# Kernel tuning notes

Measured on AMD Instinct MI355X. Metric: run time of the kernel, lower is better.

## Reference

```python
import jax, jax.numpy as jnp
import numpy as np

EPS = 1e-5

def layer_norm(x, g, b):
    m = x.mean(-1, keepdims=True)
    v = ((x - m) ** 2).mean(-1, keepdims=True)
    return (x - m) * jax.lax.rsqrt(v + EPS) * g + b

def setup_inputs() -> dict:
    key = jax.random.key(0)
    ks = jax.random.split(key, 8)
    H, T = 512, 256
    hidden_states = jax.random.normal(ks[0], (1, T, H), jnp.float32)
    U = jax.random.normal(ks[1], (H, H), jnp.float32) * 0.01
    W = jax.random.normal(ks[2], (H, H), jnp.float32) * 0.01
    a = jax.random.normal(ks[3], (H,), jnp.float32) * 0.01
    b = jax.random.normal(ks[4], (H,), jnp.float32) * 0.01
    gamma = jnp.ones((H,), jnp.float32)
    beta = jnp.zeros((H,), jnp.float32)
    targets = jax.random.randint(ks[5], (T,), 0, H)  # deterministic stand-in for torch.randint dummy targets
    return {"hidden_states": hidden_states, "U": U, "W": W, "a": a, "b": b,
            "gamma": gamma, "beta": beta, "targets": targets}

def reference(hidden_states, U, W, a, b, gamma, beta, targets):
    # batch must be 1 (torch.outer in the original requires 1-D vectors)
    h = hidden_states[0]                      # (T, H)
    z = jax.nn.relu(h @ U + a)                # (T, H) slow-path hidden

    # Per-timestep grads of CE(LayerNorm(z_t @ W + b), target_t) w.r.t. W, b
    def step_loss(z_t, tgt, W_, b_):
        y = layer_norm(z_t @ W_ + b_, gamma, beta)
        return -jax.nn.log_softmax(y)[tgt]
    grad_fn = jax.grad(step_loss, argnums=(2, 3))
    gradW, gradb = jax.vmap(grad_fn, in_axes=(0, 0, None, None))(z, targets, W, b)  # (T,H,H), (T,H)

    # W_update_t[p,q] = sum_{i<t} h_i[p] * h_t[q] * gradW_i[p,q]
    G = h[:, :, None] * gradW                 # (T, H, H)
    A = jnp.cumsum(G, axis=0) - G             # exclusive prefix sum over i
    W_upd = A * h[:, None, :]                 # (T, H, H)
    fastW = W - jnp.cumsum(W_upd, axis=0)     # cumulative fast weights per t

    # b_update_t[q] = h_t[q] * sum_{i<t} (sum_p h_i[p]) * gradb_i[q]
    c = h.sum(-1)                             # (T,)
    Bc = c[:, None] * gradb                   # (T, H)
    Bex = jnp.cumsum(Bc, axis=0) - Bc         # exclusive
    b_upd = h * Bex
    fastb = b - jnp.cumsum(b_upd, axis=0)     # (T, H)

    pre = jnp.einsum('th,thq->tq', z, fastW) + fastb
    out = layer_norm(pre, gamma, beta)        # (T, H)
    return out[None]                          # (1, T, H)
```

## Files before the change

kernel.cpp:

```cpp
#include <hip/hip_runtime.h>

#define T 256
#define H 512
#define EPSF 1e-5f

__device__ __forceinline__ float block_sum(float v, float* s4) {
    for (int o = 32; o; o >>= 1) v += __shfl_xor(v, o);
    int w = threadIdx.x >> 6;
    __syncthreads();
    if ((threadIdx.x & 63) == 0) s4[w] = v;
    __syncthreads();
    return s4[0] + s4[1] + s4[2] + s4[3];
}

__device__ __forceinline__ float block_max(float v, float* s4) {
    for (int o = 32; o; o >>= 1) v = fmaxf(v, __shfl_xor(v, o));
    int w = threadIdx.x >> 6;
    __syncthreads();
    if ((threadIdx.x & 63) == 0) s4[w] = v;
    __syncthreads();
    return fmaxf(fmaxf(s4[0], s4[1]), fmaxf(s4[2], s4[3]));
}

__device__ __forceinline__ float bsum16(float v, float* s16) {
    for (int o = 32; o; o >>= 1) v += __shfl_xor(v, o);
    int w = threadIdx.x >> 6;
    __syncthreads();
    if ((threadIdx.x & 63) == 0) s16[w] = v;
    __syncthreads();
    float r = 0.f;
    #pragma unroll
    for (int i = 0; i < 16; ++i) r += s16[i];
    return r;
}

__global__ __launch_bounds__(256) void k1(
        const float* __restrict__ h, const float* __restrict__ U,
        const float* __restrict__ a, float* __restrict__ Z,
        float* __restrict__ HZ, float* __restrict__ c) {
    int bid = blockIdx.x, tid = threadIdx.x;
    int lane = tid & 63, w = tid >> 6;
    int t0 = (bid >> 2) * 2, qt = bid & 3;
    __shared__ __align__(16) float sh[1024];
    __shared__ float2 part[3][2][64];
    ((float4*)sh)[tid] = ((const float4*)(h + t0 * H))[tid];
    __syncthreads();

    if (qt == 0 && w < 2) {
        float s = 0.f;
        #pragma unroll
        for (int j = 0; j < 8; ++j) s += sh[w * 512 + lane + j * 64];
        for (int o = 32; o; o >>= 1) s += __shfl_xor(s, o);
        if (lane == 0) c[t0 + w] = s;
    }

    int qc = qt * 64 + lane;
    const float2* U2 = (const float2*)U;
    float2 acc0 = {0.f, 0.f}, acc1 = {0.f, 0.f};
    int kbeg = w * 128;
    for (int k0 = kbeg; k0 < kbeg + 128; k0 += 8) {
        float2 bv[8];
        #pragma unroll
        for (int u = 0; u < 8; ++u) bv[u] = U2[(k0 + u) * 256 + qc];
        float a0[8], a1[8];
        #pragma unroll
        for (int u = 0; u < 8; ++u) { a0[u] = sh[k0 + u]; a1[u] = sh[512 + k0 + u]; }
        #pragma unroll
        for (int u = 0; u < 8; ++u) {
            acc0.x += a0[u] * bv[u].x; acc0.y += a0[u] * bv[u].y;
            acc1.x += a1[u] * bv[u].x; acc1.y += a1[u] * bv[u].y;
        }
    }
    if (w) { part[w - 1][0][lane] = acc0; part[w - 1][1][lane] = acc1; }
    __syncthreads();
    if (w == 0) {
        #pragma unroll
        for (int p = 0; p < 3; ++p) {
            acc0.x += part[p][0][lane].x; acc0.y += part[p][0][lane].y;
            acc1.x += part[p][1][lane].x; acc1.y += part[p][1][lane].y;
        }
        float2 av = ((const float2*)a)[qc];
        float z0x = fmaxf(acc0.x + av.x, 0.f), z0y = fmaxf(acc0.y + av.y, 0.f);
        float z1x = fmaxf(acc1.x + av.x, 0.f), z1y = fmaxf(acc1.y + av.y, 0.f);
        float2 h0 = ((float2*)sh)[qc], h1 = ((float2*)sh)[256 + qc];
        ((float2*)Z)[t0 * 256 + qc]        = make_float2(z0x, z0y);
        ((float2*)Z)[(t0 + 1) * 256 + qc]  = make_float2(z1x, z1y);
        ((float2*)HZ)[t0 * 256 + qc]       = make_float2(h0.x * z0x, h0.y * z0y);
        ((float2*)HZ)[(t0 + 1) * 256 + qc] = make_float2(h1.x * z1x, h1.y * z1y);
    }
}

__global__ __launch_bounds__(256) void k2(
        const float* __restrict__ h, const float* __restrict__ Z,
        const float* __restrict__ W, const float* __restrict__ bb,
        const float* __restrict__ HZ, const float* __restrict__ c,
        float* __restrict__ u0, float* __restrict__ Beta,
        float* __restrict__ S) {
    __shared__ __align__(16) float smem[2 * 8 * 516 + 256];
    int bid = blockIdx.x, tid = threadIdx.x;
    int lane = tid & 63, w = tid >> 6;
    if (bid < 512) {
        float* sh = smem;
        float2* part = (float2*)(smem + 1024);
        int t0 = (bid >> 2) * 2, qt = bid & 3;
        ((float4*)sh)[tid] = ((const float4*)(Z + t0 * H))[tid];
        __syncthreads();
        int qc = qt * 64 + lane;
        const float2* W2 = (const float2*)W;
        float2 acc0 = {0.f, 0.f}, acc1 = {0.f, 0.f};
        int kbeg = w * 128;
        for (int k0 = kbeg; k0 < kbeg + 128; k0 += 8) {
            float2 bv[8];
            #pragma unroll
            for (int u = 0; u < 8; ++u) bv[u] = W2[(k0 + u) * 256 + qc];
            float a0[8], a1[8];
            #pragma unroll
            for (int u = 0; u < 8; ++u) { a0[u] = sh[k0 + u]; a1[u] = sh[512 + k0 + u]; }
            #pragma unroll
            for (int u = 0; u < 8; ++u) {
                acc0.x += a0[u] * bv[u].x; acc0.y += a0[u] * bv[u].y;
                acc1.x += a1[u] * bv[u].x; acc1.y += a1[u] * bv[u].y;
            }
        }
        if (w) { part[((w - 1) * 2 + 0) * 64 + lane] = acc0; part[((w - 1) * 2 + 1) * 64 + lane] = acc1; }
        __syncthreads();
        if (w == 0) {
            #pragma unroll
            for (int p = 0; p < 3; ++p) {
                float2 p0 = part[(p * 2 + 0) * 64 + lane];
                float2 p1 = part[(p * 2 + 1) * 64 + lane];
                acc0.x += p0.x; acc0.y += p0.y;
                acc1.x += p1.x; acc1.y += p1.y;
            }
            float2 bv = ((const float2*)bb)[qc];
            ((float2*)u0)[t0 * 256 + qc]       = make_float2(acc0.x + bv.x, acc0.y + bv.y);
            ((float2*)u0)[(t0 + 1) * 256 + qc] = make_float2(acc1.x + bv.x, acc1.y + bv.y);
        }
    } else if (bid < 1040) {
        int e = bid - 512;
        int ti = (int)((sqrtf(8.f * (float)e + 1.f) - 1.f) * 0.5f);
        while ((ti + 1) * (ti + 2) / 2 <= e) ++ti;
        while (ti * (ti + 1) / 2 > e) --ti;
        int ii = e - ti * (ti + 1) / 2;
        int t0 = ti * 8, i0 = ii * 8;
        float* Zs = smem;
        float* Hs = smem + 8 * 516;
        float* red = smem + 2 * 8 * 516;
        #pragma unroll
        for (int j = 0; j < 4; ++j) {
            int idx = tid + j * 256;
            int row = idx >> 7, col4 = idx & 127;
            float4 v = ((const float4*)(Z + (t0 + row) * H))[col4];
            *(float4*)&Zs[row * 516 + col4 * 4] = v;
            float4 g = ((const float4*)(HZ + (i0 + row) * H))[col4];
            *(float4*)&Hs[row * 516 + col4 * 4] = g;
        }
        __syncthreads();
        int ks = tid >> 6, r = (tid >> 3) & 7, ci = tid & 7;
        float acc = 0.f;
        int kb = ks * 128;
        #pragma unroll 4
        for (int k0 = kb; k0 < kb + 128; k0 += 8) {
            float4 z0 = *(float4*)&Zs[r * 516 + k0];
            float4 z1 = *(float4*)&Zs[r * 516 + k0 + 4];
            float4 h0 = *(float4*)&Hs[ci * 516 + k0];
            float4 h1 = *(float4*)&Hs[ci * 516 + k0 + 4];
            acc += z0.x * h0.x + z0.y * h0.y + z0.z * h0.z + z0.w * h0.w
                 + z1.x * h1.x + z1.y * h1.y + z1.z * h1.z + z1.w * h1.w;
        }
        red[ks * 64 + r * 8 + ci] = acc;
        __syncthreads();
        if (tid < 64) {
            int r2 = tid >> 3, c2 = tid & 7;
            float v = red[tid] + red[64 + tid] + red[128 + tid] + red[192 + tid];
            int t = t0 + r2, i = i0 + c2;
            Beta[t * 256 + i] = (i < t) ? v + c[i] : 0.f;
        }
    } else {
        float* csum = smem;
        int q = (bid - 1040) * 64 + lane;
        int tbase = w * 64;
        float s = 0.f;
        for (int j = 0; j < 64; j += 8) {
            float v[8];
            #pragma unroll
            for (int u = 0; u < 8; ++u) v[u] = h[(tbase + j + u) * H + q];
            #pragma unroll
            for (int u = 0; u < 8; ++u) s += v[u];
        }
        csum[w * 64 + lane] = s;
        __syncthreads();
        float acc = 0.f;
        #pragma unroll
        for (int w2 = 0; w2 < 3; ++w2) if (w2 < w) acc += csum[w2 * 64 + lane];
        for (int j = 0; j < 64; j += 8) {
            float v[8];
            #pragma unroll
            for (int u = 0; u < 8; ++u) v[u] = h[(tbase + j + u) * H + q];
            #pragma unroll
            for (int u = 0; u < 8; ++u) { acc += v[u]; S[(tbase + j + u) * H + q] = acc; }
        }
    }
}

__global__ __launch_bounds__(256) void k3(
        const float* __restrict__ u0, const float* __restrict__ gamma,
        const float* __restrict__ beta, const int* __restrict__ targets,
        const float* __restrict__ S, float* __restrict__ D, float* __restrict__ SD) {
    __shared__ float s4[4];
    int t = blockIdx.x, tid = threadIdx.x;
    float2 uv = ((const float2*)u0)[t * 256 + tid];
    float2 gv = ((const float2*)gamma)[tid];
    float2 bv = ((const float2*)beta)[tid];

    float m = block_sum(uv.x + uv.y, s4) * (1.f / H);
    float d0 = uv.x - m, d1 = uv.y - m;
    float var = block_sum(d0 * d0 + d1 * d1, s4) * (1.f / H);
    float s = rsqrtf(var + EPSF);
    float xh0 = d0 * s, xh1 = d1 * s;
    float y0 = xh0 * gv.x + bv.x;
    float y1 = xh1 * gv.y + bv.y;

    float ymax = block_max(fmaxf(y0, y1), s4);
    float e0 = __expf(y0 - ymax), e1 = __expf(y1 - ymax);
    float Zs = block_sum(e0 + e1, s4);
    float invZ = 1.f / Zs;
    int tgt = targets[t];
    float g0 = e0 * invZ - (2 * tid == tgt ? 1.f : 0.f);
    float g1 = e1 * invZ - (2 * tid + 1 == tgt ? 1.f : 0.f);
    float gy0 = g0 * gv.x, gy1 = g1 * gv.y;

    float mgy = block_sum(gy0 + gy1, s4) * (1.f / H);
    float mgx = block_sum(gy0 * xh0 + gy1 * xh1, s4) * (1.f / H);

    float dd0 = s * (gy0 - mgy - xh0 * mgx);
    float dd1 = s * (gy1 - mgy - xh1 * mgx);
    float2 sv = ((const float2*)S)[t * 256 + tid];
    ((float2*)D)[t * 256 + tid]  = make_float2(dd0, dd1);
    ((float2*)SD)[t * 256 + tid] = make_float2(sv.x * dd0, sv.y * dd1);
}

__global__ __launch_bounds__(1024) void k4(
        const float* __restrict__ Beta, const float* __restrict__ D,
        const float* __restrict__ SD, const float* __restrict__ u0,
        const float* __restrict__ S, const float* __restrict__ gamma,
        const float* __restrict__ beta, float* __restrict__ out) {
    __shared__ float Brow[256];
    __shared__ float r1[4][512];
    __shared__ float r2[4][512];
    __shared__ float s16[16];
    int t = blockIdx.x, tid = threadIdx.x;
    if (tid < 256) Brow[tid] = Beta[t * 256 + tid];
    __syncthreads();

    int ig = tid >> 8, qc = tid & 255;
    int ibeg = ig * 64;
    int iend = min((t + 7) & ~7, ibeg + 64);
    float2 a1 = {0.f, 0.f}, a2 = {0.f, 0.f};
    const float2* D2 = (const float2*)D;
    const float2* SD2 = (const float2*)SD;
    for (int k0 = ibeg; k0 < iend; k0 += 8) {
        float2 dv[8], sv[8];
        #pragma unroll
        for (int u = 0; u < 8; ++u) {
            dv[u] = D2[(k0 + u) * 256 + qc];
            sv[u] = SD2[(k0 + u) * 256 + qc];
        }
        #pragma unroll
        for (int u = 0; u < 8; ++u) {
            float bw = Brow[k0 + u];
            a1.x += bw * dv[u].x; a1.y += bw * dv[u].y;
            a2.x += bw * sv[u].x; a2.y += bw * sv[u].y;
        }
    }
    r1[ig][2 * qc] = a1.x; r1[ig][2 * qc + 1] = a1.y;
    r2[ig][2 * qc] = a2.x; r2[ig][2 * qc + 1] = a2.y;
    __syncthreads();

    float p = 0.f;
    if (tid < 512) {
        float A1 = r1[0][tid] + r1[1][tid] + r1[2][tid] + r1[3][tid];
        float A2 = r2[0][tid] + r2[1][tid] + r2[2][tid] + r2[3][tid];
        p = u0[t * H + tid] - S[t * H + tid] * A1 + A2;
    }
    float m = bsum16(p, s16) * (1.f / H);
    float d = (tid < 512) ? p - m : 0.f;
    float var = bsum16(d * d, s16) * (1.f / H);
    float s = rsqrtf(var + EPSF);
    if (tid < 512)
        out[t * H + tid] = d * s * gamma[tid] + beta[tid];
}

extern "C" void kernel_launch(void* const* d_in, const int* in_sizes, int n_in,
                              void* d_out, int out_size, void* d_ws, size_t ws_size,
                              hipStream_t stream) {
    const float* h     = (const float*)d_in[0];
    const float* U     = (const float*)d_in[1];
    const float* W     = (const float*)d_in[2];
    const float* a     = (const float*)d_in[3];
    const float* b     = (const float*)d_in[4];
    const float* gamma = (const float*)d_in[5];
    const float* beta  = (const float*)d_in[6];
    const int*   tgt   = (const int*)d_in[7];
    float* out = (float*)d_out;

    float* ws = (float*)d_ws;
    const int TH = T * H;
    float* Z    = ws;
    float* HZ   = Z    + TH;
    float* u0   = HZ   + TH;
    float* D    = u0   + TH;
    float* SD   = D    + TH;
    float* S    = SD   + TH;
    float* c    = S    + TH;
    float* Beta = c    + T;

    k1<<<512,  256, 0, stream>>>(h, U, a, Z, HZ, c);
    k2<<<1048, 256, 0, stream>>>(h, Z, W, b, HZ, c, u0, Beta, S);
    k3<<<T,    256, 0, stream>>>(u0, gamma, beta, tgt, S, D, SD);
    k4<<<T,   1024, 0, stream>>>(Beta, D, SD, u0, S, gamma, beta, out);
}
```

Measured before the change: 114.0 us.

## Fuse four kernels into two, merging GEMMs with LayerNorm backward

Merges the U GEMM, W GEMM, layer-norm/softmax backward and the prefix-sum of h into one 1024-thread kernel working on two timesteps per block, so the z row stays in shared memory between GEMMs. The triangular Beta GEMM moves into the final kernel as per-row wave dot products, and the S*D product is computed on the fly instead of being stored. This removes two launches and several intermediate global round trips. In exchange the grid shrinks to 132 large blocks, which reduces parallelism, and each output row recomputes its Beta dot products serially.

```diff
diff --git a/kernel.cpp b/kernel.cpp
--- a/kernel.cpp
+++ b/kernel.cpp
@@ -3,24 +3,6 @@
 #define T 256
 #define H 512
 #define EPSF 1e-5f
-
-__device__ __forceinline__ float block_sum(float v, float* s4) {
-    for (int o = 32; o; o >>= 1) v += __shfl_xor(v, o);
-    int w = threadIdx.x >> 6;
-    __syncthreads();
-    if ((threadIdx.x & 63) == 0) s4[w] = v;
-    __syncthreads();
-    return s4[0] + s4[1] + s4[2] + s4[3];
-}
-
-__device__ __forceinline__ float block_max(float v, float* s4) {
-    for (int o = 32; o; o >>= 1) v = fmaxf(v, __shfl_xor(v, o));
-    int w = threadIdx.x >> 6;
-    __syncthreads();
-    if ((threadIdx.x & 63) == 0) s4[w] = v;
-    __syncthreads();
-    return fmaxf(fmaxf(s4[0], s4[1]), fmaxf(s4[2], s4[3]));
-}
 
 __device__ __forceinline__ float bsum16(float v, float* s16) {
     for (int o = 32; o; o >>= 1) v += __shfl_xor(v, o);
@@ -34,223 +16,190 @@
     return r;
 }
 
-__global__ __launch_bounds__(256) void k1(
+__device__ __forceinline__ float rowsum(float v, float* s16, int row) {
+    for (int o = 32; o; o >>= 1) v += __shfl_xor(v, o);
+    int w = threadIdx.x >> 6;
+    __syncthreads();
+    if ((threadIdx.x & 63) == 0) s16[w] = v;
+    __syncthreads();
+    float r = 0.f;
+    int base = row * 8;
+    #pragma unroll
+    for (int i = 0; i < 8; ++i) r += s16[base + i];
+    return r;
+}
+
+__device__ __forceinline__ float rowmax(float v, float* s16, int row) {
+    for (int o = 32; o; o >>= 1) v = fmaxf(v, __shfl_xor(v, o));
+    int w = threadIdx.x >> 6;
+    __syncthreads();
+    if ((threadIdx.x & 63) == 0) s16[w] = v;
+    __syncthreads();
+    float r = -1e30f;
+    int base = row * 8;
+    #pragma unroll
+    for (int i = 0; i < 8; ++i) r = fmaxf(r, s16[base + i]);
+    return r;
+}
+
+__global__ __launch_bounds__(1024) void kA(
         const float* __restrict__ h, const float* __restrict__ U,
-        const float* __restrict__ a, float* __restrict__ Z,
-        float* __restrict__ HZ, float* __restrict__ c) {
+        const float* __restrict__ W, const float* __restrict__ aa,
+        const float* __restrict__ bb, const float* __restrict__ gamma,
+        const float* __restrict__ beta, const int* __restrict__ targets,
+        float* __restrict__ Z, float* __restrict__ HZ, float* __restrict__ u0,
+        float* __restrict__ D, float* __restrict__ c, float* __restrict__ S) {
+    __shared__ __align__(16) float sh_h[1024];
+    __shared__ __align__(16) float sh_z[1024];
+    __shared__ float2 part[512];
+    __shared__ float s16[16];
     int bid = blockIdx.x, tid = threadIdx.x;
-    int lane = tid & 63, w = tid >> 6;
-    int t0 = (bid >> 2) * 2, qt = bid & 3;
-    __shared__ __align__(16) float sh[1024];
-    __shared__ float2 part[3][2][64];
-    ((float4*)sh)[tid] = ((const float4*)(h + t0 * H))[tid];
-    __syncthreads();
-
-    if (qt == 0 && w < 2) {
+
+    if (bid >= 128) {
+        __shared__ float csum[8 * 128];
+        int q = (bid - 128) * 128 + (tid & 127);
+        int tc = tid >> 7, tb = tc * 32;
         float s = 0.f;
-        #pragma unroll
-        for (int j = 0; j < 8; ++j) s += sh[w * 512 + lane + j * 64];
+        for (int j = 0; j < 32; j += 8) {
+            float v[8];
+            #pragma unroll
+            for (int u = 0; u < 8; ++u) v[u] = h[(tb + j + u) * H + q];
+            #pragma unroll
+            for (int u = 0; u < 8; ++u) s += v[u];
+        }
+        csum[tc * 128 + (tid & 127)] = s;
+        __syncthreads();
+        float acc = 0.f;
+        for (int c2 = 0; c2 < tc; ++c2) acc += csum[c2 * 128 + (tid & 127)];
+        for (int j = 0; j < 32; j += 8) {
+            float v[8];
+            #pragma unroll
+            for (int u = 0; u < 8; ++u) v[u] = h[(tb + j + u) * H + q];
+            #pragma unroll
+            for (int u = 0; u < 8; ++u) { acc += v[u]; S[(tb + j + u) * H + q] = acc; }
+        }
+        return;
+    }
+
+    int t0 = bid * 2;
+    sh_h[tid] = h[t0 * H + tid];
+    __syncthreads();
+
+    int w = tid >> 6, lane = tid & 63;
+    if (w < 2) {
+        float s = 0.f;
+        #pragma unroll
+        for (int j = 0; j < 8; ++j) s += sh_h[w * 512 + lane + j * 64];
         for (int o = 32; o; o >>= 1) s += __shfl_xor(s, o);
         if (lane == 0) c[t0 + w] = s;
     }
 
-    int qc = qt * 64 + lane;
+    int ks = tid >> 9, idx = tid & 511, r = idx >> 8, qc = idx & 255;
     const float2* U2 = (const float2*)U;
-    float2 acc0 = {0.f, 0.f}, acc1 = {0.f, 0.f};
-    int kbeg = w * 128;
-    for (int k0 = kbeg; k0 < kbeg + 128; k0 += 8) {
+    float2 acc = {0.f, 0.f};
+    int kbeg = ks * 256;
+    for (int k0 = kbeg; k0 < kbeg + 256; k0 += 8) {
         float2 bv[8];
         #pragma unroll
         for (int u = 0; u < 8; ++u) bv[u] = U2[(k0 + u) * 256 + qc];
-        float a0[8], a1[8];
-        #pragma unroll
-        for (int u = 0; u < 8; ++u) { a0[u] = sh[k0 + u]; a1[u] = sh[512 + k0 + u]; }
-        #pragma unroll
-        for (int u = 0; u < 8; ++u) {
-            acc0.x += a0[u] * bv[u].x; acc0.y += a0[u] * bv[u].y;
-            acc1.x += a1[u] * bv[u].x; acc1.y += a1[u] * bv[u].y;
-        }
-    }
-    if (w) { part[w - 1][0][lane] = acc0; part[w - 1][1][lane] = acc1; }
-    __syncthreads();
-    if (w == 0) {
-        #pragma unroll
-        for (int p = 0; p < 3; ++p) {
-            acc0.x += part[p][0][lane].x; acc0.y += part[p][0][lane].y;
-            acc1.x += part[p][1][lane].x; acc1.y += part[p][1][lane].y;
-        }
-        float2 av = ((const float2*)a)[qc];
-        float z0x = fmaxf(acc0.x + av.x, 0.f), z0y = fmaxf(acc0.y + av.y, 0.f);
-        float z1x = fmaxf(acc1.x + av.x, 0.f), z1y = fmaxf(acc1.y + av.y, 0.f);
-        float2 h0 = ((float2*)sh)[qc], h1 = ((float2*)sh)[256 + qc];
-        ((float2*)Z)[t0 * 256 + qc]        = make_float2(z0x, z0y);
-        ((float2*)Z)[(t0 + 1) * 256 + qc]  = make_float2(z1x, z1y);
-        ((float2*)HZ)[t0 * 256 + qc]       = make_float2(h0.x * z0x, h0.y * z0y);
-        ((float2*)HZ)[(t0 + 1) * 256 + qc] = make_float2(h1.x * z1x, h1.y * z1y);
-    }
-}
-
-__global__ __launch_bounds__(256) void k2(
-        const float* __restrict__ h, const float* __restrict__ Z,
-        const float* __restrict__ W, const float* __restrict__ bb,
-        const float* __restrict__ HZ, const float* __restrict__ c,
-        float* __restrict__ u0, float* __restrict__ Beta,
-        float* __restrict__ S) {
-    __shared__ __align__(16) float smem[2 * 8 * 516 + 256];
-    int bid = blockIdx.x, tid = threadIdx.x;
-    int lane = tid & 63, w = tid >> 6;
-    if (bid < 512) {
-        float* sh = smem;
-        float2* part = (float2*)(smem + 1024);
-        int t0 = (bid >> 2) * 2, qt = bid & 3;
-        ((float4*)sh)[tid] = ((const float4*)(Z + t0 * H))[tid];
-        __syncthreads();
-        int qc = qt * 64 + lane;
-        const float2* W2 = (const float2*)W;
-        float2 acc0 = {0.f, 0.f}, acc1 = {0.f, 0.f};
-        int kbeg = w * 128;
-        for (int k0 = kbeg; k0 < kbeg + 128; k0 += 8) {
-            float2 bv[8];
-            #pragma unroll
-            for (int u = 0; u < 8; ++u) bv[u] = W2[(k0 + u) * 256 + qc];
-            float a0[8], a1[8];
-            #pragma unroll
-            for (int u = 0; u < 8; ++u) { a0[u] = sh[k0 + u]; a1[u] = sh[512 + k0 + u]; }
-            #pragma unroll
-            for (int u = 0; u < 8; ++u) {
-                acc0.x += a0[u] * bv[u].x; acc0.y += a0[u] * bv[u].y;
-                acc1.x += a1[u] * bv[u].x; acc1.y += a1[u] * bv[u].y;
-            }
-        }
-        if (w) { part[((w - 1) * 2 + 0) * 64 + lane] = acc0; part[((w - 1) * 2 + 1) * 64 + lane] = acc1; }
-        __syncthreads();
-        if (w == 0) {
-            #pragma unroll
-            for (int p = 0; p < 3; ++p) {
-                float2 p0 = part[(p * 2 + 0) * 64 + lane];
-                float2 p1 = part[(p * 2 + 1) * 64 + lane];
-                acc0.x += p0.x; acc0.y += p0.y;
-                acc1.x += p1.x; acc1.y += p1.y;
-            }
-            float2 bv = ((const float2*)bb)[qc];
-            ((float2*)u0)[t0 * 256 + qc]       = make_float2(acc0.x + bv.x, acc0.y + bv.y);
-            ((float2*)u0)[(t0 + 1) * 256 + qc] = make_float2(acc1.x + bv.x, acc1.y + bv.y);
-        }
-    } else if (bid < 1040) {
-        int e = bid - 512;
-        int ti = (int)((sqrtf(8.f * (float)e + 1.f) - 1.f) * 0.5f);
-        while ((ti + 1) * (ti + 2) / 2 <= e) ++ti;
-        while (ti * (ti + 1) / 2 > e) --ti;
-        int ii = e - ti * (ti + 1) / 2;
-        int t0 = ti * 8, i0 = ii * 8;
-        float* Zs = smem;
-        float* Hs = smem + 8 * 516;
-        float* red = smem + 2 * 8 * 516;
-        #pragma unroll
-        for (int j = 0; j < 4; ++j) {
-            int idx = tid + j * 256;
-            int row = idx >> 7, col4 = idx & 127;
-            float4 v = ((const float4*)(Z + (t0 + row) * H))[col4];
-            *(float4*)&Zs[row * 516 + col4 * 4] = v;
-            float4 g = ((const float4*)(HZ + (i0 + row) * H))[col4];
-            *(float4*)&Hs[row * 516 + col4 * 4] = g;
-        }
-        __syncthreads();
-        int ks = tid >> 6, r = (tid >> 3) & 7, ci = tid & 7;
-        float acc = 0.f;
-        int kb = ks * 128;
-        #pragma unroll 4
-        for (int k0 = kb; k0 < kb + 128; k0 += 8) {
-            float4 z0 = *(float4*)&Zs[r * 516 + k0];
-            float4 z1 = *(float4*)&Zs[r * 516 + k0 + 4];
-            float4 h0 = *(float4*)&Hs[ci * 516 + k0];
-            float4 h1 = *(float4*)&Hs[ci * 516 + k0 + 4];
-            acc += z0.x * h0.x + z0.y * h0.y + z0.z * h0.z + z0.w * h0.w
-                 + z1.x * h1.x + z1.y * h1.y + z1.z * h1.z + z1.w * h1.w;
-        }
-        red[ks * 64 + r * 8 + ci] = acc;
-        __syncthreads();
-        if (tid < 64) {
-            int r2 = tid >> 3, c2 = tid & 7;
-            float v = red[tid] + red[64 + tid] + red[128 + tid] + red[192 + tid];
-            int t = t0 + r2, i = i0 + c2;
-            Beta[t * 256 + i] = (i < t) ? v + c[i] : 0.f;
-        }
-    } else {
-        float* csum = smem;
-        int q = (bid - 1040) * 64 + lane;
-        int tbase = w * 64;
-        float s = 0.f;
-        for (int j = 0; j < 64; j += 8) {
-            float v[8];
-            #pragma unroll
-            for (int u = 0; u < 8; ++u) v[u] = h[(tbase + j + u) * H + q];
-            #pragma unroll
-            for (int u = 0; u < 8; ++u) s += v[u];
-        }
-        csum[w * 64 + lane] = s;
-        __syncthreads();
-        float acc = 0.f;
-        #pragma unroll
-        for (int w2 = 0; w2 < 3; ++w2) if (w2 < w) acc += csum[w2 * 64 + lane];
-        for (int j = 0; j < 64; j += 8) {
-            float v[8];
-            #pragma unroll
-            for (int u = 0; u < 8; ++u) v[u] = h[(tbase + j + u) * H + q];
-            #pragma unroll
-            for (int u = 0; u < 8; ++u) { acc += v[u]; S[(tbase + j + u) * H + q] = acc; }
-        }
-    }
-}
-
-__global__ __launch_bounds__(256) void k3(
-        const float* __restrict__ u0, const float* __restrict__ gamma,
-        const float* __restrict__ beta, const int* __restrict__ targets,
-        const float* __restrict__ S, float* __restrict__ D, float* __restrict__ SD) {
-    __shared__ float s4[4];
-    int t = blockIdx.x, tid = threadIdx.x;
-    float2 uv = ((const float2*)u0)[t * 256 + tid];
-    float2 gv = ((const float2*)gamma)[tid];
-    float2 bv = ((const float2*)beta)[tid];
-
-    float m = block_sum(uv.x + uv.y, s4) * (1.f / H);
-    float d0 = uv.x - m, d1 = uv.y - m;
-    float var = block_sum(d0 * d0 + d1 * d1, s4) * (1.f / H);
+        float av[8];
+        #pragma unroll
+        for (int u = 0; u < 8; ++u) av[u] = sh_h[r * 512 + k0 + u];
+        #pragma unroll
+        for (int u = 0; u < 8; ++u) { acc.x += av[u] * bv[u].x; acc.y += av[u] * bv[u].y; }
+    }
+    if (ks == 1) part[idx] = acc;
+    __syncthreads();
+    if (ks == 0) {
+        float2 p = part[idx];
+        acc.x += p.x; acc.y += p.y;
+        float2 av2 = ((const float2*)aa)[qc];
+        float zx = fmaxf(acc.x + av2.x, 0.f), zy = fmaxf(acc.y + av2.y, 0.f);
+        sh_z[r * 512 + 2 * qc] = zx; sh_z[r * 512 + 2 * qc + 1] = zy;
+        ((float2*)Z)[(t0 + r) * 256 + qc] = make_float2(zx, zy);
+        float hx = sh_h[r * 512 + 2 * qc], hy = sh_h[r * 512 + 2 * qc + 1];
+        ((float2*)HZ)[(t0 + r) * 256 + qc] = make_float2(hx * zx, hy * zy);
+    }
+    __syncthreads();
+
+    const float2* W2 = (const float2*)W;
+    float2 acc2 = {0.f, 0.f};
+    for (int k0 = kbeg; k0 < kbeg + 256; k0 += 8) {
+        float2 bv[8];
+        #pragma unroll
+        for (int u = 0; u < 8; ++u) bv[u] = W2[(k0 + u) * 256 + qc];
+        float av[8];
+        #pragma unroll
+        for (int u = 0; u < 8; ++u) av[u] = sh_z[r * 512 + k0 + u];
+        #pragma unroll
+        for (int u = 0; u < 8; ++u) { acc2.x += av[u] * bv[u].x; acc2.y += av[u] * bv[u].y; }
+    }
+    if (ks == 1) part[idx] = acc2;
+    __syncthreads();
+    if (ks == 0) {
+        float2 p = part[idx];
+        acc2.x += p.x; acc2.y += p.y;
+        float2 bv2 = ((const float2*)bb)[qc];
+        float ux = acc2.x + bv2.x, uy = acc2.y + bv2.y;
+        sh_h[r * 512 + 2 * qc] = ux; sh_h[r * 512 + 2 * qc + 1] = uy;
+        ((float2*)u0)[(t0 + r) * 256 + qc] = make_float2(ux, uy);
+    }
+    __syncthreads();
+
+    int row = tid >> 9, col = tid & 511;
+    int t = t0 + row;
+    float uv = sh_h[row * 512 + col];
+    float gv = gamma[col], bev = beta[col];
+    float m = rowsum(uv, s16, row) * (1.f / H);
+    float d = uv - m;
+    float var = rowsum(d * d, s16, row) * (1.f / H);
     float s = rsqrtf(var + EPSF);
-    float xh0 = d0 * s, xh1 = d1 * s;
-    float y0 = xh0 * gv.x + bv.x;
-    float y1 = xh1 * gv.y + bv.y;
-
-    float ymax = block_max(fmaxf(y0, y1), s4);
-    float e0 = __expf(y0 - ymax), e1 = __expf(y1 - ymax);
-    float Zs = block_sum(e0 + e1, s4);
-    float invZ = 1.f / Zs;
-    int tgt = targets[t];
-    float g0 = e0 * invZ - (2 * tid == tgt ? 1.f : 0.f);
-    float g1 = e1 * invZ - (2 * tid + 1 == tgt ? 1.f : 0.f);
-    float gy0 = g0 * gv.x, gy1 = g1 * gv.y;
-
-    float mgy = block_sum(gy0 + gy1, s4) * (1.f / H);
-    float mgx = block_sum(gy0 * xh0 + gy1 * xh1, s4) * (1.f / H);
-
-    float dd0 = s * (gy0 - mgy - xh0 * mgx);
-    float dd1 = s * (gy1 - mgy - xh1 * mgx);
-    float2 sv = ((const float2*)S)[t * 256 + tid];
-    ((float2*)D)[t * 256 + tid]  = make_float2(dd0, dd1);
-    ((float2*)SD)[t * 256 + tid] = make_float2(sv.x * dd0, sv.y * dd1);
-}
-
-__global__ __launch_bounds__(1024) void k4(
-        const float* __restrict__ Beta, const float* __restrict__ D,
-        const float* __restrict__ SD, const float* __restrict__ u0,
-        const float* __restrict__ S, const float* __restrict__ gamma,
-        const float* __restrict__ beta, float* __restrict__ out) {
+    float xh = d * s;
+    float y = xh * gv + bev;
+    float ymax = rowmax(y, s16, row);
+    float e = __expf(y - ymax);
+    float Zs = rowsum(e, s16, row);
+    int tg = targets[t];
+    float g = e / Zs - (col == tg ? 1.f : 0.f);
+    float gy = g * gv;
+    float mgy = rowsum(gy, s16, row) * (1.f / H);
+    float mgx = rowsum(gy * xh, s16, row) * (1.f / H);
+    D[t * H + col] = s * (gy - mgy - xh * mgx);
+}
+
+__global__ __launch_bounds__(1024) void kB(
+        const float* __restrict__ Z, const float* __restrict__ HZ,
+        const float* __restrict__ c, const float* __restrict__ D,
+        const float* __restrict__ S, const float* __restrict__ u0,
+        const float* __restrict__ gamma, const float* __restrict__ beta,
+        float* __restrict__ out) {
+    __shared__ __align__(16) float zrow[512];
+    __shared__ float cs[256];
     __shared__ float Brow[256];
     __shared__ float r1[4][512];
     __shared__ float r2[4][512];
     __shared__ float s16[16];
     int t = blockIdx.x, tid = threadIdx.x;
-    if (tid < 256) Brow[tid] = Beta[t * 256 + tid];
+
+    if (tid < 512) zrow[tid] = Z[t * H + tid];
+    else if (tid < 768) cs[tid - 512] = c[tid - 512];
+    else Brow[tid - 768] = 0.f;
+    __syncthreads();
+
+    int w = tid >> 6, lane = tid & 63;
+    const float2* HZ2 = (const float2*)HZ;
+    const float2* z2 = (const float2*)zrow;
+    for (int i = w; i < t; i += 16) {
+        float acc = 0.f;
+        #pragma unroll
+        for (int k = 0; k < 4; ++k) {
+            float2 hv = HZ2[i * 256 + lane + k * 64];
+            float2 zv = z2[lane + k * 64];
+            acc += hv.x * zv.x + hv.y * zv.y;
+        }
+        for (int o = 32; o; o >>= 1) acc += __shfl_xor(acc, o);
+        if (lane == 0) Brow[i] = acc + cs[i];
+    }
     __syncthreads();
 
     int ig = tid >> 8, qc = tid & 255;
@@ -258,19 +207,19 @@
     int iend = min((t + 7) & ~7, ibeg + 64);
     float2 a1 = {0.f, 0.f}, a2 = {0.f, 0.f};
     const float2* D2 = (const float2*)D;
-    const float2* SD2 = (const float2*)SD;
+    const float2* S2 = (const float2*)S;
     for (int k0 = ibeg; k0 < iend; k0 += 8) {
         float2 dv[8], sv[8];
         #pragma unroll
         for (int u = 0; u < 8; ++u) {
             dv[u] = D2[(k0 + u) * 256 + qc];
-            sv[u] = SD2[(k0 + u) * 256 + qc];
+            sv[u] = S2[(k0 + u) * 256 + qc];
         }
         #pragma unroll
         for (int u = 0; u < 8; ++u) {
             float bw = Brow[k0 + u];
-            a1.x += bw * dv[u].x; a1.y += bw * dv[u].y;
-            a2.x += bw * sv[u].x; a2.y += bw * sv[u].y;
+            a1.x += bw * dv[u].x;          a1.y += bw * dv[u].y;
+            a2.x += bw * sv[u].x * dv[u].x; a2.y += bw * sv[u].y * dv[u].y;
         }
     }
     r1[ig][2 * qc] = a1.x; r1[ig][2 * qc + 1] = a1.y;
@@ -306,17 +255,13 @@
 
     float* ws = (float*)d_ws;
     const int TH = T * H;
-    float* Z    = ws;
-    float* HZ   = Z    + TH;
-    float* u0   = HZ   + TH;
-    float* D    = u0   + TH;
-    float* SD   = D    + TH;
-    float* S    = SD   + TH;
-    float* c    = S    + TH;
-    float* Beta = c    + T;
-
-    k1<<<512,  256, 0, stream>>>(h, U, a, Z, HZ, c);
-    k2<<<1048, 256, 0, stream>>>(h, Z, W, b, HZ, c, u0, Beta, S);
-    k3<<<T,    256, 0, stream>>>(u0, gamma, beta, tgt, S, D, SD);
-    k4<<<T,   1024, 0, stream>>>(Beta, D, SD, u0, S, gamma, beta, out);
-}
+    float* Z  = ws;
+    float* HZ = Z  + TH;
+    float* u0 = HZ + TH;
+    float* D  = u0 + TH;
+    float* S  = D  + TH;
+    float* c  = S  + TH;
+
+    kA<<<132, 1024, 0, stream>>>(h, U, W, a, b, gamma, beta, tgt, Z, HZ, u0, D, c, S);
+    kB<<<T,   1024, 0, stream>>>(Z, HZ, c, D, S, u0, gamma, beta, out);
+}
```

Result: slower. 161.4 us (+41.5%).
